# Performance work log

Hardware: AMD Instinct MI355X
Metric: run time of the kernel (lower is better)

The kernel has to match this reference:

```python
import jax, jax.numpy as jnp
import numpy as np

N, E, F_NODE, F_EDGE, EMB, HID, NGRAPH = 10000, 30000, 32, 8, 64, 16, 64


def _edge_mlp(e, w1, b1, w2, b2):
    # Seq(Linear(F_EDGE,16), ReLU, Linear(16, in*out))
    return jax.nn.relu(e @ w1 + b1) @ w2 + b2


def setup_inputs() -> dict:
    key = jax.random.key(0)
    ks = jax.random.split(key, 24)
    s = lambda k, shape, fan: jax.random.normal(k, shape, jnp.float32) * (1.0 / np.sqrt(fan))
    inp = {
        "x_p": jax.random.normal(ks[0], (N, F_NODE), jnp.float32),
        "x_d": jax.random.normal(ks[1], (1, F_NODE), jnp.float32),
        "edge_attr_p": jax.random.uniform(ks[2], (E, F_EDGE), jnp.float32),
        "edge_attr_d": jax.random.uniform(ks[3], (1, F_EDGE), jnp.float32),
        "edge_index_p": jax.random.randint(ks[4], (2, E), 0, N, jnp.int32),
        "x_p_batch": jnp.sort(jax.random.randint(ks[5], (N,), 0, NGRAPH, jnp.int32)),
        # edge MLP of first conv: F_EDGE -> 16 -> F_NODE*EMB
        "nn0_w1": s(ks[6], (F_EDGE, HID), F_EDGE), "nn0_b1": jnp.zeros((HID,), jnp.float32),
        "nn0_w2": s(ks[7], (HID, F_NODE * EMB), HID), "nn0_b2": jnp.zeros((F_NODE * EMB,), jnp.float32),
        # shared edge MLP of later convs: F_EDGE -> 16 -> EMB*EMB
        "nn1_w1": s(ks[8], (F_EDGE, HID), F_EDGE), "nn1_b1": jnp.zeros((HID,), jnp.float32),
        "nn1_w2": s(ks[9], (HID, EMB * EMB), HID), "nn1_b2": jnp.zeros((EMB * EMB,), jnp.float32),
        # per-conv root weights and biases
        "root0": s(ks[10], (F_NODE, EMB), F_NODE), "bias0": jnp.zeros((EMB,), jnp.float32),
        "root1": s(ks[11], (EMB, EMB), EMB), "bias1": jnp.zeros((EMB,), jnp.float32),
        "root2": s(ks[12], (EMB, EMB), EMB), "bias2": jnp.zeros((EMB,), jnp.float32),
        # head: Linear(EMB,EMB) then Linear(EMB,1), no activation between (per source)
        "lin0_w": s(ks[13], (EMB, EMB), EMB), "lin0_b": jnp.zeros((EMB,), jnp.float32),
        "lin1_w": s(ks[14], (EMB, 1), EMB), "lin1_b": jnp.zeros((1,), jnp.float32),
    }
    return inp


def reference(x_p, x_d, edge_attr_p, edge_attr_d,
              nn0_w1, nn0_b1, nn0_w2, nn0_b2,
              nn1_w1, nn1_b1, nn1_w2, nn1_b2,
              root0, bias0, root1, bias1, root2, bias2,
              lin0_w, lin0_b, lin1_w, lin1_b,
              edge_index_p, x_p_batch):
    src, dst = edge_index_p[0], edge_index_p[1]

    # conv 0: edge-conditioned weights [E, F_NODE, EMB]
    W0 = _edge_mlp(edge_attr_p, nn0_w1, nn0_b1, nn0_w2, nn0_b2).reshape(E, F_NODE, EMB)
    msg = jnp.einsum('ei,eio->eo', x_p[src], W0)
    agg = jax.ops.segment_sum(msg, dst, num_segments=N)
    x = jax.nn.relu(agg + x_p @ root0 + bias0)

    # convs 1..L-1 share the same edge MLP (same nn1 instance in source), so
    # the per-edge weight matrices [E, EMB, EMB] are identical: compute once.
    W1 = _edge_mlp(edge_attr_p, nn1_w1, nn1_b1, nn1_w2, nn1_b2).reshape(E, EMB, EMB)
    for root, bias in ((root1, bias1), (root2, bias2)):
        msg = jnp.einsum('ei,eio->eo', x[src], W1)
        agg = jax.ops.segment_sum(msg, dst, num_segments=N)
        x = jax.nn.relu(agg + x @ root + bias)

    # global max pool over graphs, dropout is identity in eval mode
    pooled = jax.ops.segment_max(x, x_p_batch, num_segments=NGRAPH)
    h = pooled @ lin0_w + lin0_b
    out = h @ lin1_w + lin1_b  # [NGRAPH, 1]
    return out
```

## Files before the change

### kernel.cpp

```cpp
#include <hip/hip_runtime.h>
#include <hip/hip_bf16.h>

#define N_NODES 10000
#define N_EDGES 30000
#define F_NODE  32
#define F_EDGE  8
#define EMB     64
#define HID     16
#define NGRAPH  64
#define NBUCK   625
#define CAP     128
#define NCOL    1088
#define ROWW    514
#define XTS     72

typedef __attribute__((ext_vector_type(8))) short short8;
typedef __attribute__((ext_vector_type(4))) float f32x4;

__device__ __forceinline__ unsigned short f2b(float f) {
    __hip_bfloat16 h = __float2bfloat16(f);
    return __builtin_bit_cast(unsigned short, h);
}

struct P {
    const float *x_p, *ea;
    const int *src, *dst, *batch;
    const float *nn0_w1, *nn0_b1, *nn0_w2, *nn0_b2;
    const float *nn1_w1, *nn1_b1, *nn1_w2, *nn1_b2;
    const float *root0, *bias0, *root1, *bias1, *root2, *bias2;
    const float *lin0_w, *lin0_b, *lin1_w, *lin1_b;
    float *out;
    int *cnt, *metap;
    float *A1p;
    unsigned short *W2p0, *W2p1;
    float *AGGa, *AGGb, *X0, *X1;
};

__global__ void __launch_bounds__(256) k_prep(P p) {
    int b = blockIdx.x, t = threadIdx.x;
    if (b < 136) {
        int i = b * 256 + t;
        if (i >= NCOL * F_NODE) return;
        int rt = i >> 5, k = i & 31;
        float v;
        if (rt < 1024) {
            int T = rt >> 4, lr = rt & 15;
            int o = ((T >> 4) << 4) + lr, h = T & 15;
            v = p.nn0_w2[h * (F_NODE * EMB) + k * EMB + o];
        } else {
            v = p.nn0_b2[k * EMB + (rt - 1024)];
        }
        p.W2p0[i] = f2b(v);
    } else if (b < 408) {
        int i = (b - 136) * 256 + t;
        if (i >= NCOL * EMB) return;
        int rt = i >> 6, k = i & 63;
        float v;
        if (rt < 1024) {
            int T = rt >> 4, lr = rt & 15;
            int o = ((T >> 4) << 4) + lr, h = T & 15;
            v = p.nn1_w2[h * (EMB * EMB) + k * EMB + o];
        } else {
            v = p.nn1_b2[k * EMB + (rt - 1024)];
        }
        p.W2p1[i] = f2b(v);
    } else {
        int idx = (b - 408) * 256 + t;
        float4* Z = (float4*)p.AGGa;
        const float4 z4 = {0.f, 0.f, 0.f, 0.f};
        for (int i = idx; i < (N_NODES * EMB) / 4; i += 160 * 256) Z[i] = z4;
    }
}

template <int CONV>
__global__ void __launch_bounds__(512) k_fused(P p) {
    constexpr int K = (CONV == 0) ? F_NODE : EMB;
    __shared__ unsigned short U2[16 * 2 * ROWW];
    __shared__ float XB_l[16][65];
    __shared__ unsigned short Xt[16][XTS];
    __shared__ float A0l[CAP][HID];
    __shared__ int lds_e[CAP];
    __shared__ int meta_l[CAP];
    __shared__ int lcnt;
    const int b = blockIdx.x, t = threadIdx.x;
    const int n0 = b * 16;
    const int w = t >> 6, l = t & 63;
    const int lrow = l & 15, lk4 = l >> 4;
    int cnt = 0;

    if (CONV == 0) {
        float4* Zb = (float4*)(p.AGGb + (size_t)n0 * EMB);
        const float4 z4 = {0.f, 0.f, 0.f, 0.f};
        for (int idx = t; idx < 16 * EMB / 4; idx += 512) Zb[idx] = z4;
        if (t == 0) lcnt = 0;
        __syncthreads();
        const int4* s4 = (const int4*)p.src;
        for (int i = t; i < N_EDGES / 4; i += 512) {
            int4 v = s4[i];
            int e0 = i * 4;
            if ((v.x >> 4) == b) { int sl = atomicAdd(&lcnt, 1); if (sl < CAP) lds_e[sl] = ((e0    ) << 4) | (v.x & 15); }
            if ((v.y >> 4) == b) { int sl = atomicAdd(&lcnt, 1); if (sl < CAP) lds_e[sl] = ((e0 + 1) << 4) | (v.y & 15); }
            if ((v.z >> 4) == b) { int sl = atomicAdd(&lcnt, 1); if (sl < CAP) lds_e[sl] = ((e0 + 2) << 4) | (v.z & 15); }
            if ((v.w >> 4) == b) { int sl = atomicAdd(&lcnt, 1); if (sl < CAP) lds_e[sl] = ((e0 + 3) << 4) | (v.w & 15); }
        }
        __syncthreads();
        cnt = lcnt; if (cnt > CAP) cnt = CAP;
        if (t == 0) p.cnt[b] = cnt;
        if (t < cnt) {
            int pk = lds_e[t];
            int e = pk >> 4, sloc = pk & 15;
            int mt = p.dst[e] * 16 + sloc;
            meta_l[t] = mt;
            p.metap[(size_t)b * CAP + t] = mt;
            const float4* ea4 = (const float4*)(p.ea + (size_t)e * F_EDGE);
            float4 ef0 = ea4[0], ef1 = ea4[1];
            float fv[F_EDGE] = {ef0.x, ef0.y, ef0.z, ef0.w, ef1.x, ef1.y, ef1.z, ef1.w};
            float a1v[HID];
#pragma unroll
            for (int h = 0; h < HID; h++) {
                float s0 = p.nn0_b1[h], s1 = p.nn1_b1[h];
#pragma unroll
                for (int i = 0; i < F_EDGE; i++) {
                    s0 += fv[i] * p.nn0_w1[i * HID + h];
                    s1 += fv[i] * p.nn1_w1[i * HID + h];
                }
                A0l[t][h] = fmaxf(s0, 0.f);
                a1v[h] = fmaxf(s1, 0.f);
            }
            float4* A1g = (float4*)(p.A1p + ((size_t)b * CAP + t) * HID);
#pragma unroll
            for (int j = 0; j < 4; j++)
                A1g[j] = float4{a1v[4 * j], a1v[4 * j + 1], a1v[4 * j + 2], a1v[4 * j + 3]};
        }
    }

    if (CONV > 0) {
        const float* aggIn = (CONV == 1) ? p.AGGa : p.AGGb;
        const float* rt = (CONV == 1) ? p.root0 : p.root1;
        const float* bs = (CONV == 1) ? p.bias0 : p.bias1;
        constexpr int IN = (CONV == 1) ? F_NODE : EMB;
        for (int idx = t; idx < 16 * 64; idx += 512) {
            int j = idx >> 6, o = idx & 63;
            int n = n0 + j;
            const float* xr = (CONV == 1) ? (p.x_p + (size_t)n * IN)
                                          : (p.X0 + (size_t)n * IN);
            float s0 = aggIn[n * EMB + o] + bs[o];
            float s1 = 0.f, s2 = 0.f, s3 = 0.f;
#pragma unroll
            for (int i = 0; i < IN; i += 4) {
                s0 = fmaf(xr[i + 0], rt[(i + 0) * EMB + o], s0);
                s1 = fmaf(xr[i + 1], rt[(i + 1) * EMB + o], s1);
                s2 = fmaf(xr[i + 2], rt[(i + 2) * EMB + o], s2);
                s3 = fmaf(xr[i + 3], rt[(i + 3) * EMB + o], s3);
            }
            float sv = fmaxf((s0 + s1) + (s2 + s3), 0.f);
            Xt[j][o] = f2b(sv);
            if (CONV == 1) { p.X0[n * EMB + o] = sv; p.AGGa[n * EMB + o] = 0.f; }
            else           { p.X1[n * EMB + o] = sv; }
        }
        __syncthreads();
        cnt = p.cnt[b];
    }

    short8 afr[K / 32];
    if (CONV == 0) {
        const float* xp = p.x_p + (size_t)(n0 + lrow) * F_NODE + lk4 * 8;
#pragma unroll
        for (int q = 0; q < 8; q++) afr[0][q] = (short)f2b(xp[q]);
    } else {
#pragma unroll
        for (int kk = 0; kk < K / 32; kk++)
            afr[kk] = *reinterpret_cast<const short8*>(&Xt[lrow][kk * 32 + lk4 * 8]);
    }
    const unsigned short* W2p = (CONV == 0) ? p.W2p0 : p.W2p1;
    for (int i = 0; i <= 8; i++) {
        int T = w + 8 * i;
        if (T >= 68) break;
        short8 bfr[K / 32];
#pragma unroll
        for (int kk = 0; kk < K / 32; kk++)
            bfr[kk] = *reinterpret_cast<const short8*>(
                W2p + (size_t)(T * 16 + lrow) * K + kk * 32 + lk4 * 8);
        f32x4 acc = {0.f, 0.f, 0.f, 0.f};
#pragma unroll
        for (int kk = 0; kk < K / 32; kk++)
            acc = __builtin_amdgcn_mfma_f32_16x16x32_bf16(afr[kk], bfr[kk], acc, 0, 0, 0);
        if (T < 64) {
            int h = T & 15, hw = h >> 1, hb = h & 1;
            int ob = ((T >> 4) << 4) + lrow;
#pragma unroll
            for (int r = 0; r < 4; r++)
                U2[(lk4 * 4 + r) * (2 * ROWW) + hw * 128 + ob * 2 + hb] = f2b(acc[r]);
        } else {
            int col = (T - 64) * 16 + lrow;
#pragma unroll
            for (int r = 0; r < 4; r++)
                XB_l[lk4 * 4 + r][col] = acc[r];
        }
    }
    __syncthreads();

    float* aggOut = (CONV == 1) ? p.AGGb : p.AGGa;
    const size_t base = (size_t)b * CAP;
    const int o = l;
#pragma unroll 2
    for (int qi = w; qi < cnt; qi += 8) {
        int q = __builtin_amdgcn_readfirstlane(qi);
        int mt;
        float av[HID];
        if (CONV == 0) {
            mt = meta_l[q];
            const float4* a4 = (const float4*)A0l[q];
            float4 u0 = a4[0], u1 = a4[1], u2 = a4[2], u3 = a4[3];
            av[0]=u0.x; av[1]=u0.y; av[2]=u0.z; av[3]=u0.w;
            av[4]=u1.x; av[5]=u1.y; av[6]=u1.z; av[7]=u1.w;
            av[8]=u2.x; av[9]=u2.y; av[10]=u2.z; av[11]=u2.w;
            av[12]=u3.x; av[13]=u3.y; av[14]=u3.z; av[15]=u3.w;
        } else {
            mt = p.metap[base + q];
            const float* Ae = p.A1p + (base + q) * HID;
#pragma unroll
            for (int h = 0; h < HID; h++) av[h] = Ae[h];
        }
        int sloc = mt & 15, dd = mt >> 4;
        const unsigned* up = reinterpret_cast<const unsigned*>(U2) + sloc * ROWW + o;
        float m0 = XB_l[sloc][o], m1 = 0.f;
#define ACC2(dst_, wrd, h)                                                            \
        dst_ = fmaf(__builtin_bit_cast(float, (unsigned)(wrd) << 16), av[h], dst_);   \
        dst_ = fmaf(__builtin_bit_cast(float, (unsigned)(wrd) & 0xffff0000u), av[h + 1], dst_);
#pragma unroll
        for (int hh = 0; hh < 4; hh++) {
            unsigned ua = up[hh * 64];
            unsigned ub = up[(hh + 4) * 64];
            ACC2(m0, ua, 2 * hh)
            ACC2(m1, ub, 2 * (hh + 4))
        }
#undef ACC2
        atomicAdd(&aggOut[(size_t)dd * EMB + o], m0 + m1);
    }
}

__global__ void __launch_bounds__(512) k_tail(P p) {
    __shared__ unsigned pool[EMB];
    const int g = blockIdx.x, t = threadIdx.x;
    const int w = t >> 6, o = t & 63;
    if (t < EMB) pool[t] = 0u;
    __syncthreads();
    int lo = 0, hi = N_NODES;
    while (lo < hi) { int mid = (lo + hi) >> 1; if (p.batch[mid] < g) lo = mid + 1; else hi = mid; }
    int lo2 = lo, hi2 = N_NODES;
    while (lo2 < hi2) { int mid = (lo2 + hi2) >> 1; if (p.batch[mid] < g + 1) lo2 = mid + 1; else hi2 = mid; }
    const float b2 = p.bias2[o];
    float rcol[EMB];
#pragma unroll
    for (int i = 0; i < EMB; i++) rcol[i] = p.root2[i * EMB + o];
    float mx = 0.f;
    for (int nn = lo + w; nn < lo2; nn += 8) {
        int n = __builtin_amdgcn_readfirstlane(nn);
        const float* xr = p.X1 + (size_t)n * EMB;
        float s0 = p.AGGa[(size_t)n * EMB + o] + b2;
        float s1 = 0.f, s2 = 0.f, s3 = 0.f;
#pragma unroll
        for (int i = 0; i < EMB; i += 4) {
            s0 = fmaf(xr[i + 0], rcol[i + 0], s0);
            s1 = fmaf(xr[i + 1], rcol[i + 1], s1);
            s2 = fmaf(xr[i + 2], rcol[i + 2], s2);
            s3 = fmaf(xr[i + 3], rcol[i + 3], s3);
        }
        mx = fmaxf(mx, fmaxf((s0 + s1) + (s2 + s3), 0.f));
    }
    atomicMax(&pool[o], __float_as_uint(mx));
    __syncthreads();
    if (t < EMB) {
        int o2 = t;
        float h = p.lin0_b[o2];
#pragma unroll 8
        for (int oo = 0; oo < EMB; oo++)
            h += __uint_as_float(pool[oo]) * p.lin0_w[oo * EMB + o2];
        float v = h * p.lin1_w[o2];
#pragma unroll
        for (int off = 32; off; off >>= 1) v += __shfl_down(v, off, 64);
        if (o2 == 0) p.out[g] = v + p.lin1_b[0];
    }
}

extern "C" void kernel_launch(void* const* d_in, const int* in_sizes, int n_in,
                              void* d_out, int out_size, void* d_ws, size_t ws_size,
                              hipStream_t stream) {
    P p;
    p.x_p    = (const float*)d_in[0];
    p.ea     = (const float*)d_in[2];
    const int* eidx = (const int*)d_in[4];
    p.src    = eidx;
    p.dst    = eidx + N_EDGES;
    p.batch  = (const int*)d_in[5];
    p.nn0_w1 = (const float*)d_in[6];  p.nn0_b1 = (const float*)d_in[7];
    p.nn0_w2 = (const float*)d_in[8];  p.nn0_b2 = (const float*)d_in[9];
    p.nn1_w1 = (const float*)d_in[10]; p.nn1_b1 = (const float*)d_in[11];
    p.nn1_w2 = (const float*)d_in[12]; p.nn1_b2 = (const float*)d_in[13];
    p.root0  = (const float*)d_in[14]; p.bias0  = (const float*)d_in[15];
    p.root1  = (const float*)d_in[16]; p.bias1  = (const float*)d_in[17];
    p.root2  = (const float*)d_in[18]; p.bias2  = (const float*)d_in[19];
    p.lin0_w = (const float*)d_in[20]; p.lin0_b = (const float*)d_in[21];
    p.lin1_w = (const float*)d_in[22]; p.lin1_b = (const float*)d_in[23];
    p.out    = (float*)d_out;

    char* ws = (char*)d_ws;
    p.AGGa   = (float*)ws;          ws += (size_t)N_NODES * EMB * 4;
    p.AGGb   = (float*)ws;          ws += (size_t)N_NODES * EMB * 4;
    p.cnt    = (int*)ws;            ws += 2560;
    p.metap  = (int*)ws;            ws += (size_t)NBUCK * CAP * 4;
    p.A1p    = (float*)ws;          ws += (size_t)NBUCK * CAP * HID * 4;
    p.W2p0   = (unsigned short*)ws; ws += (size_t)NCOL * F_NODE * 2;
    p.W2p1   = (unsigned short*)ws; ws += (size_t)NCOL * EMB * 2;
    p.X0     = (float*)ws;          ws += (size_t)N_NODES * EMB * 4;
    p.X1     = (float*)ws;          ws += (size_t)N_NODES * EMB * 4;

    k_prep<<<568, 256, 0, stream>>>(p);
    k_fused<0><<<NBUCK, 512, 0, stream>>>(p);
    k_fused<1><<<NBUCK, 512, 0, stream>>>(p);
    k_fused<2><<<NBUCK, 512, 0, stream>>>(p);
    k_tail<<<NGRAPH, 512, 0, stream>>>(p);
}
```

Measured before the change: 213.6 us.

## Fold root-weight matmul into MFMA tile loop and atomically pre-add into aggregation

```diff
diff --git a/kernel.cpp b/kernel.cpp
--- a/kernel.cpp
+++ b/kernel.cpp
@@ -32,8 +32,8 @@
     float *out;
     int *cnt, *metap;
     float *A1p;
-    unsigned short *W2p0, *W2p1;
-    float *AGGa, *AGGb, *X0, *X1;
+    unsigned short *W2p0, *W2p1, *RTW0, *RTW1, *RTW2;
+    float *AGGa, *AGGb;
 };
 
 __global__ void __launch_bounds__(256) k_prep(P p) {
@@ -64,8 +64,20 @@
             v = p.nn1_b2[k * EMB + (rt - 1024)];
         }
         p.W2p1[i] = f2b(v);
+    } else if (b < 416) {
+        int i = (b - 408) * 256 + t;
+        int col = i >> 5, k = i & 31;
+        p.RTW0[i] = f2b(p.root0[k * EMB + col]);
+    } else if (b < 432) {
+        int i = (b - 416) * 256 + t;
+        int col = i >> 6, k = i & 63;
+        p.RTW1[i] = f2b(p.root1[k * EMB + col]);
+    } else if (b < 448) {
+        int i = (b - 432) * 256 + t;
+        int col = i >> 6, k = i & 63;
+        p.RTW2[i] = f2b(p.root2[k * EMB + col]);
     } else {
-        int idx = (b - 408) * 256 + t;
+        int idx = (b - 448) * 256 + t;
         float4* Z = (float4*)p.AGGa;
         const float4 z4 = {0.f, 0.f, 0.f, 0.f};
         for (int i = idx; i < (N_NODES * EMB) / 4; i += 160 * 256) Z[i] = z4;
@@ -136,27 +148,12 @@
 
     if (CONV > 0) {
         const float* aggIn = (CONV == 1) ? p.AGGa : p.AGGb;
-        const float* rt = (CONV == 1) ? p.root0 : p.root1;
-        const float* bs = (CONV == 1) ? p.bias0 : p.bias1;
-        constexpr int IN = (CONV == 1) ? F_NODE : EMB;
         for (int idx = t; idx < 16 * 64; idx += 512) {
             int j = idx >> 6, o = idx & 63;
             int n = n0 + j;
-            const float* xr = (CONV == 1) ? (p.x_p + (size_t)n * IN)
-                                          : (p.X0 + (size_t)n * IN);
-            float s0 = aggIn[n * EMB + o] + bs[o];
-            float s1 = 0.f, s2 = 0.f, s3 = 0.f;
-#pragma unroll
-            for (int i = 0; i < IN; i += 4) {
-                s0 = fmaf(xr[i + 0], rt[(i + 0) * EMB + o], s0);
-                s1 = fmaf(xr[i + 1], rt[(i + 1) * EMB + o], s1);
-                s2 = fmaf(xr[i + 2], rt[(i + 2) * EMB + o], s2);
-                s3 = fmaf(xr[i + 3], rt[(i + 3) * EMB + o], s3);
-            }
-            float sv = fmaxf((s0 + s1) + (s2 + s3), 0.f);
+            float sv = fmaxf(aggIn[n * EMB + o], 0.f);
             Xt[j][o] = f2b(sv);
-            if (CONV == 1) { p.X0[n * EMB + o] = sv; p.AGGa[n * EMB + o] = 0.f; }
-            else           { p.X1[n * EMB + o] = sv; }
+            if (CONV == 1) p.AGGa[n * EMB + o] = 0.f;
         }
         __syncthreads();
         cnt = p.cnt[b];
@@ -173,14 +170,25 @@
             afr[kk] = *reinterpret_cast<const short8*>(&Xt[lrow][kk * 32 + lk4 * 8]);
     }
     const unsigned short* W2p = (CONV == 0) ? p.W2p0 : p.W2p1;
-    for (int i = 0; i <= 8; i++) {
+    const unsigned short* RTW = (CONV == 0) ? p.RTW0 : ((CONV == 1) ? p.RTW1 : p.RTW2);
+    const float* bias = (CONV == 0) ? p.bias0 : ((CONV == 1) ? p.bias1 : p.bias2);
+    float* aggOut = (CONV == 1) ? p.AGGb : p.AGGa;
+#pragma unroll
+    for (int i = 0; i < 9; i++) {
         int T = w + 8 * i;
-        if (T >= 68) break;
         short8 bfr[K / 32];
-#pragma unroll
-        for (int kk = 0; kk < K / 32; kk++)
-            bfr[kk] = *reinterpret_cast<const short8*>(
-                W2p + (size_t)(T * 16 + lrow) * K + kk * 32 + lk4 * 8);
+        if (T < 68) {
+#pragma unroll
+            for (int kk = 0; kk < K / 32; kk++)
+                bfr[kk] = *reinterpret_cast<const short8*>(
+                    W2p + (size_t)(T * 16 + lrow) * K + kk * 32 + lk4 * 8);
+        } else {
+            int col = (T - 68) * 16 + lrow;
+#pragma unroll
+            for (int kk = 0; kk < K / 32; kk++)
+                bfr[kk] = *reinterpret_cast<const short8*>(
+                    RTW + (size_t)col * K + kk * 32 + lk4 * 8);
+        }
         f32x4 acc = {0.f, 0.f, 0.f, 0.f};
 #pragma unroll
         for (int kk = 0; kk < K / 32; kk++)
@@ -191,16 +199,21 @@
 #pragma unroll
             for (int r = 0; r < 4; r++)
                 U2[(lk4 * 4 + r) * (2 * ROWW) + hw * 128 + ob * 2 + hb] = f2b(acc[r]);
-        } else {
+        } else if (T < 68) {
             int col = (T - 64) * 16 + lrow;
 #pragma unroll
             for (int r = 0; r < 4; r++)
                 XB_l[lk4 * 4 + r][col] = acc[r];
+        } else {
+            int col = (T - 68) * 16 + lrow;
+            float bo = bias[col];
+#pragma unroll
+            for (int r = 0; r < 4; r++)
+                atomicAdd(&aggOut[(size_t)(n0 + lk4 * 4 + r) * EMB + col], acc[r] + bo);
         }
     }
     __syncthreads();
 
-    float* aggOut = (CONV == 1) ? p.AGGb : p.AGGa;
     const size_t base = (size_t)b * CAP;
     const int o = l;
 #pragma unroll 2
@@ -250,24 +263,10 @@
     while (lo < hi) { int mid = (lo + hi) >> 1; if (p.batch[mid] < g) lo = mid + 1; else hi = mid; }
     int lo2 = lo, hi2 = N_NODES;
     while (lo2 < hi2) { int mid = (lo2 + hi2) >> 1; if (p.batch[mid] < g + 1) lo2 = mid + 1; else hi2 = mid; }
-    const float b2 = p.bias2[o];
-    float rcol[EMB];
-#pragma unroll
-    for (int i = 0; i < EMB; i++) rcol[i] = p.root2[i * EMB + o];
     float mx = 0.f;
     for (int nn = lo + w; nn < lo2; nn += 8) {
         int n = __builtin_amdgcn_readfirstlane(nn);
-        const float* xr = p.X1 + (size_t)n * EMB;
-        float s0 = p.AGGa[(size_t)n * EMB + o] + b2;
-        float s1 = 0.f, s2 = 0.f, s3 = 0.f;
-#pragma unroll
-        for (int i = 0; i < EMB; i += 4) {
-            s0 = fmaf(xr[i + 0], rcol[i + 0], s0);
-            s1 = fmaf(xr[i + 1], rcol[i + 1], s1);
-            s2 = fmaf(xr[i + 2], rcol[i + 2], s2);
-            s3 = fmaf(xr[i + 3], rcol[i + 3], s3);
-        }
-        mx = fmaxf(mx, fmaxf((s0 + s1) + (s2 + s3), 0.f));
+        mx = fmaxf(mx, fmaxf(p.AGGa[(size_t)n * EMB + o], 0.f));
     }
     atomicMax(&pool[o], __float_as_uint(mx));
     __syncthreads();
@@ -313,10 +312,11 @@
     p.A1p    = (float*)ws;          ws += (size_t)NBUCK * CAP * HID * 4;
     p.W2p0   = (unsigned short*)ws; ws += (size_t)NCOL * F_NODE * 2;
     p.W2p1   = (unsigned short*)ws; ws += (size_t)NCOL * EMB * 2;
-    p.X0     = (float*)ws;          ws += (size_t)N_NODES * EMB * 4;
-    p.X1     = (float*)ws;          ws += (size_t)N_NODES * EMB * 4;
-
-    k_prep<<<568, 256, 0, stream>>>(p);
+    p.RTW0   = (unsigned short*)ws; ws += (size_t)EMB * F_NODE * 2;
+    p.RTW1   = (unsigned short*)ws; ws += (size_t)EMB * EMB * 2;
+    p.RTW2   = (unsigned short*)ws; ws += (size_t)EMB * EMB * 2;
+
+    k_prep<<<608, 256, 0, stream>>>(p);
     k_fused<0><<<NBUCK, 512, 0, stream>>>(p);
     k_fused<1><<<NBUCK, 512, 0, stream>>>(p);
     k_fused<2><<<NBUCK, 512, 0, stream>>>(p);
```

After: 179.6 us, median of 2. 1.19x faster.
